# Kernel optimization log

Measured on AMD Instinct MI355X. Metric: run time of the kernel, lower is better.

The kernel has to match this reference:

```python
import jax, jax.numpy as jnp
import numpy as np

NUM_PROB_BINS = 15
NUM_CLASSES = 8
NEIGHBORHOOD_WIDTH = 3
NUM_NEIGHBOR_CLASSES = NEIGHBORHOOD_WIDTH ** 2  # 9
B, H, W = 16, 512, 512


def _bin_index(x, nbins):
    # Uniform bins on [0, 1]: bin_idx = floor(x * nbins), last bin closed at 1.0.
    idx = jnp.floor(x * nbins).astype(jnp.int32)
    return jnp.clip(idx, 0, nbins - 1)


def setup_inputs() -> dict:
    key = jax.random.key(0)
    k1, k2 = jax.random.split(key)
    logits = jax.random.normal(k1, (B, NUM_CLASSES, H, W), dtype=jnp.float32)
    # Precomputed calibration frequency table: [num_classes, num_neighbor_bins, num_prob_bins]
    val_freqs = jax.random.uniform(k2, (NUM_CLASSES, NUM_NEIGHBOR_CLASSES, NUM_PROB_BINS), dtype=jnp.float32)
    return {"logits": logits, "val_freqs": val_freqs}


def reference(logits, val_freqs):
    probs = jax.nn.softmax(logits, axis=1)  # [B, C, H, W]
    kw = NEIGHBORHOOD_WIDTH
    # agg_neighbors_preds (soft, class_wise): mean prob over kw x kw spatial neighborhood.
    neigh_mean = jax.lax.reduce_window(
        probs, 0.0, jax.lax.add,
        window_dimensions=(1, 1, kw, kw),
        window_strides=(1, 1, 1, 1),
        padding='SAME',
    ) / float(kw * kw)
    loc_bin = _bin_index(neigh_mean, NUM_NEIGHBOR_CLASSES)  # [B,C,H,W] int32 in [0,9)
    prob_bin = _bin_index(probs, NUM_PROB_BINS)             # [B,C,H,W] int32 in [0,15)
    # The nested class/neighbor-bin loops + masked assignment collapse to one fused gather:
    cls_idx = jnp.arange(NUM_CLASSES, dtype=jnp.int32)[None, :, None, None]
    calibrated = val_freqs[cls_idx, loc_bin, prob_bin]       # [B,C,H,W]
    # normalize=True branch
    s = jnp.sum(calibrated, axis=1, keepdims=True)
    s = jnp.where(s == 0, jnp.ones_like(s), s)
    return calibrated / s
```

## Files before the change

### kernel.cpp

```cpp
#include <hip/hip_runtime.h>
#include <math.h>

constexpr int NPB = 15;
constexpr int NC  = 8;
constexpr int NNB = 9;
constexpr int Bn  = 16;
constexpr int Hc  = 512;
constexpr int Wc  = 512;

constexpr int TX = 64, TY = 32;
constexpr int HX = TX + 2;
constexpr int HY = TY + 2;
constexpr int NT = 1024;
constexpr int GX = Wc / TX;
constexpr int GY = Hc / TY;
constexpr int NBLK = GX * GY * Bn;
constexpr int NHALO = HX * HY;

typedef float f32x2 __attribute__((ext_vector_type(2)));

__device__ __forceinline__ void exp4_cr(const float* a, float* o) {
    double r[4], p[4];
    int    k[4];
    #pragma unroll
    for (int j = 0; j < 4; j++) {
        const double d = (double)a[j];
        double kd = rint(d * 2.8853900817779268);
        k[j] = (int)kd;
        r[j] = fma(kd, -0.34657359027997265, d);
        p[j] = 2.48015873015873016e-5;
    }
    #pragma unroll
    for (int j = 0; j < 4; j++) p[j] = fma(p[j], r[j], 1.98412698412698413e-4);
    #pragma unroll
    for (int j = 0; j < 4; j++) p[j] = fma(p[j], r[j], 1.38888888888888889e-3);
    #pragma unroll
    for (int j = 0; j < 4; j++) p[j] = fma(p[j], r[j], 8.33333333333333333e-3);
    #pragma unroll
    for (int j = 0; j < 4; j++) p[j] = fma(p[j], r[j], 4.16666666666666666e-2);
    #pragma unroll
    for (int j = 0; j < 4; j++) p[j] = fma(p[j], r[j], 1.66666666666666667e-1);
    #pragma unroll
    for (int j = 0; j < 4; j++) p[j] = fma(p[j], r[j], 0.5);
    #pragma unroll
    for (int j = 0; j < 4; j++) p[j] = fma(p[j], r[j], 1.0);
    #pragma unroll
    for (int j = 0; j < 4; j++) p[j] = fma(p[j], r[j], 1.0);
    #pragma unroll
    for (int j = 0; j < 4; j++) {
        double v = (k[j] & 1) ? p[j] * 1.4142135623730951 : p[j];
        long long bits = __double_as_longlong(v) + ((long long)(k[j] >> 1) << 52);
        o[j] = (float)__longlong_as_double(bits);
    }
}

__device__ __forceinline__ double rcp64(float s) {
    double dS = (double)s;
    double r  = (double)__builtin_amdgcn_rcpf(s);
    r = r * fma(-dS, r, 2.0);
    r = r * fma(-dS, r, 2.0);
    return r;
}

__global__ __launch_bounds__(NT, 8)
void nectar_kernel(const float* __restrict__ logits,
                   const float* __restrict__ vf,
                   float* __restrict__ out)
{
    __shared__ __align__(16) float sP[NC][HY][HX];
    __shared__ float sVF[NC * NNB * NPB];

    const int tid = threadIdx.x;

    const int h    = blockIdx.x;
    const int sg   = h >> 8;
    const int xcd  = h & 7;
    const int slot = (h >> 3) & 31;
    const int sem  = (sg << 8) + (xcd << 5) + slot;

    const int bx = sem & (GX - 1);
    const int by = (sem >> 3) & (GY - 1);
    const int b  = sem >> 7;
    const int x0 = bx * TX;
    const int y0 = by * TY;

    const size_t plane = (size_t)Hc * Wc;
    const float* src = logits + (size_t)b * NC * plane;

    if (tid < NC * NNB * NPB) sVF[tid] = vf[tid];

    int ly_[3], lx_[3];
    bool img_[3];
    unsigned voff_[3];
    const bool has2 = tid < (NHALO - 2 * NT);

    #pragma unroll
    for (int t = 0; t < 3; t++) {
        const int i  = tid + t * NT;
        const int ly = (int)((unsigned)i / (unsigned)HX);
        const int lx = i - ly * HX;
        const int gy = y0 + ly - 1;
        const int gx = x0 + lx - 1;
        ly_[t]  = ly;
        lx_[t]  = lx;
        img_[t] = ((unsigned)gy < (unsigned)Hc) && ((unsigned)gx < (unsigned)Wc);
        const int gyc = gy < 0 ? 0 : (gy > Hc - 1 ? Hc - 1 : gy);
        const int gxc = gx < 0 ? 0 : (gx > Wc - 1 ? Wc - 1 : gx);
        voff_[t] = (unsigned)(gyc * Wc + gxc);
    }

    float v0[NC], v1[NC];
    #pragma unroll
    for (int c = 0; c < NC; c++) {
        const float* bc = src + (size_t)c * plane;
        v0[c] = bc[voff_[0]];
        v1[c] = bc[voff_[1]];
    }

    {
        float m = v0[0];
        #pragma unroll
        for (int c = 1; c < NC; c++) m = fmaxf(m, v0[c]);
        float d[NC], e[NC];
        #pragma unroll
        for (int c = 0; c < NC; c++) d[c] = v0[c] - m;
        exp4_cr(d, e);
        exp4_cr(d + 4, e + 4);
        float S = 0.0f;
        #pragma unroll
        for (int c = 0; c < NC; c++) S = S + e[c];
        double rS = rcp64(S);
        rS = img_[0] ? rS : 0.0;
        #pragma unroll
        for (int c = 0; c < NC; c++)
            sP[c][ly_[0]][lx_[0]] = (float)((double)e[c] * rS);
    }

    float v2[NC];
    if (has2) {
        #pragma unroll
        for (int c = 0; c < NC; c++) {
            const float* bc = src + (size_t)c * plane;
            v2[c] = bc[voff_[2]];
        }
    }

    {
        float m = v1[0];
        #pragma unroll
        for (int c = 1; c < NC; c++) m = fmaxf(m, v1[c]);
        float d[NC], e[NC];
        #pragma unroll
        for (int c = 0; c < NC; c++) d[c] = v1[c] - m;
        exp4_cr(d, e);
        exp4_cr(d + 4, e + 4);
        float S = 0.0f;
        #pragma unroll
        for (int c = 0; c < NC; c++) S = S + e[c];
        double rS = rcp64(S);
        rS = img_[1] ? rS : 0.0;
        #pragma unroll
        for (int c = 0; c < NC; c++)
            sP[c][ly_[1]][lx_[1]] = (float)((double)e[c] * rS);
    }

    if (has2) {
        float m = v2[0];
        #pragma unroll
        for (int c = 1; c < NC; c++) m = fmaxf(m, v2[c]);
        float d[NC], e[NC];
        #pragma unroll
        for (int c = 0; c < NC; c++) d[c] = v2[c] - m;
        exp4_cr(d, e);
        exp4_cr(d + 4, e + 4);
        float S = 0.0f;
        #pragma unroll
        for (int c = 0; c < NC; c++) S = S + e[c];
        double rS = rcp64(S);
        rS = img_[2] ? rS : 0.0;
        #pragma unroll
        for (int c = 0; c < NC; c++)
            sP[c][ly_[2]][lx_[2]] = (float)((double)e[c] * rS);
    }
    __syncthreads();

    const int lx2 = (tid & 31) * 2;
    const int oy  = tid >> 5;
    const int gx2 = x0 + lx2;
    const int gy  = y0 + oy;

    const double C9 = 0.1111111111111111111;

    float calL[NC], calR[NC];
    float s0 = 0.0f, s1 = 0.0f;
    #pragma unroll
    for (int c = 0; c < NC; c++) {
        const float* base = &sP[c][oy][lx2];
        f32x2 u0 = *(const f32x2*)(base);
        f32x2 w0 = *(const f32x2*)(base + 2);
        f32x2 u1 = *(const f32x2*)(base + HX);
        f32x2 w1 = *(const f32x2*)(base + HX + 2);
        f32x2 u2 = *(const f32x2*)(base + 2 * HX);
        f32x2 w2 = *(const f32x2*)(base + 2 * HX + 2);
        float a0 = ((((((((u0.x + u0.y) + w0.x) + u1.x) + u1.y) + w1.x) + u2.x) + u2.y) + w2.x);
        float a1 = ((((((((u0.y + w0.x) + w0.y) + u1.y) + w1.x) + w1.y) + u2.y) + w2.x) + w2.y);

        float nm0 = (float)((double)a0 * C9);
        float nm1 = (float)((double)a1 * C9);
        int lb0 = (int)(nm0 * 9.0f);
        int lb1 = (int)(nm1 * 9.0f);
        lb0 = lb0 > NNB - 1 ? NNB - 1 : lb0;
        lb1 = lb1 > NNB - 1 ? NNB - 1 : lb1;
        int pb0 = (int)(u1.y * 15.0f);
        int pb1 = (int)(w1.x * 15.0f);
        pb0 = pb0 > NPB - 1 ? NPB - 1 : pb0;
        pb1 = pb1 > NPB - 1 ? NPB - 1 : pb1;
        calL[c] = sVF[(c * NNB + lb0) * NPB + pb0];
        calR[c] = sVF[(c * NNB + lb1) * NPB + pb1];
        s0 = s0 + calL[c];
        s1 = s1 + calR[c];
    }
    if (s0 == 0.0f) s0 = 1.0f;
    if (s1 == 0.0f) s1 = 1.0f;

    float q0 = __builtin_amdgcn_rcpf(s0);
    q0 = q0 * fmaf(-s0, q0, 2.0f);
    float q1 = __builtin_amdgcn_rcpf(s1);
    q1 = q1 * fmaf(-s1, q1, 2.0f);

    const unsigned voff_out = (unsigned)(gy * Wc + gx2);
    #pragma unroll
    for (int c = 0; c < NC; c++) {
        float* oc = out + ((size_t)b * NC + (size_t)c) * plane;
        f32x2 o;
        o.x = calL[c] * q0;
        o.y = calR[c] * q1;
        __builtin_nontemporal_store(o, (f32x2*)(oc + voff_out));
    }
}

extern "C" void kernel_launch(void* const* d_in, const int* in_sizes, int n_in,
                              void* d_out, int out_size, void* d_ws, size_t ws_size,
                              hipStream_t stream) {
    const float* logits = (const float*)d_in[0];
    const float* vf     = (const float*)d_in[1];
    float* out          = (float*)d_out;

    nectar_kernel<<<dim3(NBLK), dim3(NT), 0, stream>>>(logits, vf, out);
}
```

Measured before the change: 227.6 us.

## Make blocks persistent over four horizontal tiles with prefetch of next tile's logits

Each block now loops over four consecutive 64-wide tiles in a row band instead of handling one tile, cutting the grid from 2048 to 512 blocks. The loads of the next tile's halo logits are issued right after the barrier, so they overlap with the stencil, gather and store phase of the current tile. The val_freqs table is loaded into shared memory once per block instead of once per tile. In exchange there is an extra barrier per tile, fewer blocks to hide latency, and halo columns are still recomputed for each tile.

```diff
diff --git a/kernel.cpp b/kernel.cpp
--- a/kernel.cpp
+++ b/kernel.cpp
@@ -12,9 +12,8 @@
 constexpr int HX = TX + 2;
 constexpr int HY = TY + 2;
 constexpr int NT = 1024;
-constexpr int GX = Wc / TX;
-constexpr int GY = Hc / TY;
-constexpr int NBLK = GX * GY * Bn;
+constexpr int TPB = 4;
+constexpr int NBLK = 512;
 constexpr int NHALO = HX * HY;
 
 typedef float f32x2 __attribute__((ext_vector_type(2)));
@@ -72,170 +71,190 @@
 
     const int tid = threadIdx.x;
 
-    const int h    = blockIdx.x;
-    const int sg   = h >> 8;
-    const int xcd  = h & 7;
-    const int slot = (h >> 3) & 31;
-    const int sem  = (sg << 8) + (xcd << 5) + slot;
-
-    const int bx = sem & (GX - 1);
-    const int by = (sem >> 3) & (GY - 1);
-    const int b  = sem >> 7;
-    const int x0 = bx * TX;
-    const int y0 = by * TY;
+    const int h   = blockIdx.x;
+    const int sem = (h & 7) * 64 + (h >> 3);
+    const int b   = sem >> 5;
+    const int rr  = sem & 31;
+    const int by  = rr >> 1;
+    const int g   = rr & 1;
+    const int y0  = by * TY;
 
     const size_t plane = (size_t)Hc * Wc;
     const float* src = logits + (size_t)b * NC * plane;
 
-    if (tid < NC * NNB * NPB) sVF[tid] = vf[tid];
+    for (int i = tid; i < NC * NNB * NPB; i += NT) sVF[i] = vf[i];
 
     int ly_[3], lx_[3];
-    bool img_[3];
-    unsigned voff_[3];
+    unsigned rowo_[3];
+    bool imy_[3];
     const bool has2 = tid < (NHALO - 2 * NT);
-
     #pragma unroll
     for (int t = 0; t < 3; t++) {
         const int i  = tid + t * NT;
         const int ly = (int)((unsigned)i / (unsigned)HX);
         const int lx = i - ly * HX;
         const int gy = y0 + ly - 1;
-        const int gx = x0 + lx - 1;
         ly_[t]  = ly;
         lx_[t]  = lx;
-        img_[t] = ((unsigned)gy < (unsigned)Hc) && ((unsigned)gx < (unsigned)Wc);
+        imy_[t] = (unsigned)gy < (unsigned)Hc;
         const int gyc = gy < 0 ? 0 : (gy > Hc - 1 ? Hc - 1 : gy);
+        rowo_[t] = (unsigned)(gyc * Wc);
+    }
+
+    const int lx2 = (tid & 31) * 2;
+    const int oy  = tid >> 5;
+    const unsigned rowout = (unsigned)((y0 + oy) * Wc);
+    const double C9 = 0.1111111111111111111;
+
+    auto task_off = [&](int t, int x0, bool& im) -> unsigned {
+        const int gx  = x0 + lx_[t] - 1;
         const int gxc = gx < 0 ? 0 : (gx > Wc - 1 ? Wc - 1 : gx);
-        voff_[t] = (unsigned)(gyc * Wc + gxc);
-    }
+        im = imy_[t] && ((unsigned)gx < (unsigned)Wc);
+        return rowo_[t] + (unsigned)gxc;
+    };
+
+    const int x0base = g * (TX * TPB);
 
     float v0[NC], v1[NC];
-    #pragma unroll
-    for (int c = 0; c < NC; c++) {
-        const float* bc = src + (size_t)c * plane;
-        v0[c] = bc[voff_[0]];
-        v1[c] = bc[voff_[1]];
-    }
-
+    bool  im0, im1;
     {
-        float m = v0[0];
-        #pragma unroll
-        for (int c = 1; c < NC; c++) m = fmaxf(m, v0[c]);
-        float d[NC], e[NC];
-        #pragma unroll
-        for (int c = 0; c < NC; c++) d[c] = v0[c] - m;
-        exp4_cr(d, e);
-        exp4_cr(d + 4, e + 4);
-        float S = 0.0f;
-        #pragma unroll
-        for (int c = 0; c < NC; c++) S = S + e[c];
-        double rS = rcp64(S);
-        rS = img_[0] ? rS : 0.0;
-        #pragma unroll
-        for (int c = 0; c < NC; c++)
-            sP[c][ly_[0]][lx_[0]] = (float)((double)e[c] * rS);
-    }
-
-    float v2[NC];
-    if (has2) {
+        const unsigned voa = task_off(0, x0base, im0);
+        const unsigned vob = task_off(1, x0base, im1);
         #pragma unroll
         for (int c = 0; c < NC; c++) {
             const float* bc = src + (size_t)c * plane;
-            v2[c] = bc[voff_[2]];
-        }
-    }
-
-    {
-        float m = v1[0];
+            v0[c] = bc[voa];
+            v1[c] = bc[vob];
+        }
+    }
+
+    for (int j = 0; j < TPB; ++j) {
+        const int xj = x0base + j * TX;
+
+        {
+            float m = v0[0];
+            #pragma unroll
+            for (int c = 1; c < NC; c++) m = fmaxf(m, v0[c]);
+            float d[NC], e[NC];
+            #pragma unroll
+            for (int c = 0; c < NC; c++) d[c] = v0[c] - m;
+            exp4_cr(d, e);
+            exp4_cr(d + 4, e + 4);
+            float S = 0.0f;
+            #pragma unroll
+            for (int c = 0; c < NC; c++) S = S + e[c];
+            double rS = rcp64(S);
+            rS = im0 ? rS : 0.0;
+            #pragma unroll
+            for (int c = 0; c < NC; c++)
+                sP[c][ly_[0]][lx_[0]] = (float)((double)e[c] * rS);
+        }
+
+        float v2[NC];
+        bool  im2 = false;
+        if (has2) {
+            const unsigned voc = task_off(2, xj, im2);
+            #pragma unroll
+            for (int c = 0; c < NC; c++) v2[c] = (src + (size_t)c * plane)[voc];
+        }
+
+        {
+            float m = v1[0];
+            #pragma unroll
+            for (int c = 1; c < NC; c++) m = fmaxf(m, v1[c]);
+            float d[NC], e[NC];
+            #pragma unroll
+            for (int c = 0; c < NC; c++) d[c] = v1[c] - m;
+            exp4_cr(d, e);
+            exp4_cr(d + 4, e + 4);
+            float S = 0.0f;
+            #pragma unroll
+            for (int c = 0; c < NC; c++) S = S + e[c];
+            double rS = rcp64(S);
+            rS = im1 ? rS : 0.0;
+            #pragma unroll
+            for (int c = 0; c < NC; c++)
+                sP[c][ly_[1]][lx_[1]] = (float)((double)e[c] * rS);
+        }
+
+        if (has2) {
+            float m = v2[0];
+            #pragma unroll
+            for (int c = 1; c < NC; c++) m = fmaxf(m, v2[c]);
+            float d[NC], e[NC];
+            #pragma unroll
+            for (int c = 0; c < NC; c++) d[c] = v2[c] - m;
+            exp4_cr(d, e);
+            exp4_cr(d + 4, e + 4);
+            float S = 0.0f;
+            #pragma unroll
+            for (int c = 0; c < NC; c++) S = S + e[c];
+            double rS = rcp64(S);
+            rS = im2 ? rS : 0.0;
+            #pragma unroll
+            for (int c = 0; c < NC; c++)
+                sP[c][ly_[2]][lx_[2]] = (float)((double)e[c] * rS);
+        }
+        __syncthreads();
+
+        if (j + 1 < TPB) {
+            const unsigned voa = task_off(0, xj + TX, im0);
+            const unsigned vob = task_off(1, xj + TX, im1);
+            #pragma unroll
+            for (int c = 0; c < NC; c++) {
+                const float* bc = src + (size_t)c * plane;
+                v0[c] = bc[voa];
+                v1[c] = bc[vob];
+            }
+        }
+
+        float calL[NC], calR[NC];
+        float s0 = 0.0f, s1 = 0.0f;
         #pragma unroll
-        for (int c = 1; c < NC; c++) m = fmaxf(m, v1[c]);
-        float d[NC], e[NC];
+        for (int c = 0; c < NC; c++) {
+            const float* base = &sP[c][oy][lx2];
+            f32x2 u0 = *(const f32x2*)(base);
+            f32x2 w0 = *(const f32x2*)(base + 2);
+            f32x2 u1 = *(const f32x2*)(base + HX);
+            f32x2 w1 = *(const f32x2*)(base + HX + 2);
+            f32x2 u2 = *(const f32x2*)(base + 2 * HX);
+            f32x2 w2 = *(const f32x2*)(base + 2 * HX + 2);
+            float a0 = ((((((((u0.x + u0.y) + w0.x) + u1.x) + u1.y) + w1.x) + u2.x) + u2.y) + w2.x);
+            float a1 = ((((((((u0.y + w0.x) + w0.y) + u1.y) + w1.x) + w1.y) + u2.y) + w2.x) + w2.y);
+
+            float nm0 = (float)((double)a0 * C9);
+            float nm1 = (float)((double)a1 * C9);
+            int lb0 = (int)(nm0 * 9.0f);
+            int lb1 = (int)(nm1 * 9.0f);
+            lb0 = lb0 > NNB - 1 ? NNB - 1 : lb0;
+            lb1 = lb1 > NNB - 1 ? NNB - 1 : lb1;
+            int pb0 = (int)(u1.y * 15.0f);
+            int pb1 = (int)(w1.x * 15.0f);
+            pb0 = pb0 > NPB - 1 ? NPB - 1 : pb0;
+            pb1 = pb1 > NPB - 1 ? NPB - 1 : pb1;
+            calL[c] = sVF[(c * NNB + lb0) * NPB + pb0];
+            calR[c] = sVF[(c * NNB + lb1) * NPB + pb1];
+            s0 = s0 + calL[c];
+            s1 = s1 + calR[c];
+        }
+        if (s0 == 0.0f) s0 = 1.0f;
+        if (s1 == 0.0f) s1 = 1.0f;
+
+        float q0 = __builtin_amdgcn_rcpf(s0);
+        q0 = q0 * fmaf(-s0, q0, 2.0f);
+        float q1 = __builtin_amdgcn_rcpf(s1);
+        q1 = q1 * fmaf(-s1, q1, 2.0f);
+
+        const unsigned voff_out = rowout + (unsigned)(xj + lx2);
         #pragma unroll
-        for (int c = 0; c < NC; c++) d[c] = v1[c] - m;
-        exp4_cr(d, e);
-        exp4_cr(d + 4, e + 4);
-        float S = 0.0f;
-        #pragma unroll
-        for (int c = 0; c < NC; c++) S = S + e[c];
-        double rS = rcp64(S);
-        rS = img_[1] ? rS : 0.0;
-        #pragma unroll
-        for (int c = 0; c < NC; c++)
-            sP[c][ly_[1]][lx_[1]] = (float)((double)e[c] * rS);
-    }
-
-    if (has2) {
-        float m = v2[0];
-        #pragma unroll
-        for (int c = 1; c < NC; c++) m = fmaxf(m, v2[c]);
-        float d[NC], e[NC];
-        #pragma unroll
-        for (int c = 0; c < NC; c++) d[c] = v2[c] - m;
-        exp4_cr(d, e);
-        exp4_cr(d + 4, e + 4);
-        float S = 0.0f;
-        #pragma unroll
-        for (int c = 0; c < NC; c++) S = S + e[c];
-        double rS = rcp64(S);
-        rS = img_[2] ? rS : 0.0;
-        #pragma unroll
-        for (int c = 0; c < NC; c++)
-            sP[c][ly_[2]][lx_[2]] = (float)((double)e[c] * rS);
-    }
-    __syncthreads();
-
-    const int lx2 = (tid & 31) * 2;
-    const int oy  = tid >> 5;
-    const int gx2 = x0 + lx2;
-    const int gy  = y0 + oy;
-
-    const double C9 = 0.1111111111111111111;
-
-    float calL[NC], calR[NC];
-    float s0 = 0.0f, s1 = 0.0f;
-    #pragma unroll
-    for (int c = 0; c < NC; c++) {
-        const float* base = &sP[c][oy][lx2];
-        f32x2 u0 = *(const f32x2*)(base);
-        f32x2 w0 = *(const f32x2*)(base + 2);
-        f32x2 u1 = *(const f32x2*)(base + HX);
-        f32x2 w1 = *(const f32x2*)(base + HX + 2);
-        f32x2 u2 = *(const f32x2*)(base + 2 * HX);
-        f32x2 w2 = *(const f32x2*)(base + 2 * HX + 2);
-        float a0 = ((((((((u0.x + u0.y) + w0.x) + u1.x) + u1.y) + w1.x) + u2.x) + u2.y) + w2.x);
-        float a1 = ((((((((u0.y + w0.x) + w0.y) + u1.y) + w1.x) + w1.y) + u2.y) + w2.x) + w2.y);
-
-        float nm0 = (float)((double)a0 * C9);
-        float nm1 = (float)((double)a1 * C9);
-        int lb0 = (int)(nm0 * 9.0f);
-        int lb1 = (int)(nm1 * 9.0f);
-        lb0 = lb0 > NNB - 1 ? NNB - 1 : lb0;
-        lb1 = lb1 > NNB - 1 ? NNB - 1 : lb1;
-        int pb0 = (int)(u1.y * 15.0f);
-        int pb1 = (int)(w1.x * 15.0f);
-        pb0 = pb0 > NPB - 1 ? NPB - 1 : pb0;
-        pb1 = pb1 > NPB - 1 ? NPB - 1 : pb1;
-        calL[c] = sVF[(c * NNB + lb0) * NPB + pb0];
-        calR[c] = sVF[(c * NNB + lb1) * NPB + pb1];
-        s0 = s0 + calL[c];
-        s1 = s1 + calR[c];
-    }
-    if (s0 == 0.0f) s0 = 1.0f;
-    if (s1 == 0.0f) s1 = 1.0f;
-
-    float q0 = __builtin_amdgcn_rcpf(s0);
-    q0 = q0 * fmaf(-s0, q0, 2.0f);
-    float q1 = __builtin_amdgcn_rcpf(s1);
-    q1 = q1 * fmaf(-s1, q1, 2.0f);
-
-    const unsigned voff_out = (unsigned)(gy * Wc + gx2);
-    #pragma unroll
-    for (int c = 0; c < NC; c++) {
-        float* oc = out + ((size_t)b * NC + (size_t)c) * plane;
-        f32x2 o;
-        o.x = calL[c] * q0;
-        o.y = calR[c] * q1;
-        __builtin_nontemporal_store(o, (f32x2*)(oc + voff_out));
+        for (int c = 0; c < NC; c++) {
+            float* oc = out + ((size_t)b * NC + (size_t)c) * plane;
+            f32x2 o;
+            o.x = calL[c] * q0;
+            o.y = calR[c] * q1;
+            __builtin_nontemporal_store(o, (f32x2*)(oc + voff_out));
+        }
+        __syncthreads();
     }
 }
 
```

After: 270.3 us. 1.19x slower.
